# Performance work log

Hardware: AMD Instinct MI355X
Metric: run time of the kernel (lower is better)

## Reference

```python
import jax, jax.numpy as jnp
import numpy as np

# RosaAttention config constants
H = 16       # num_rosa_heads
KV = 4       # num_rosa_key_value_heads
QKB = 64     # num_rosa_query_key_bits
VB = 64      # num_rosa_value_bits
HID = 2048   # hidden_size
TAU = 1.0    # temperature buffer


def setup_inputs() -> dict:
    key = jax.random.key(0)
    ks = jax.random.split(key, 8)
    B, S = 2, 2048
    sc = 0.02
    return {
        "x": jax.random.normal(ks[0], (B, S, HID), jnp.float32),
        "attention_mask": jnp.ones((B, S), jnp.int32),
        "Wq": jax.random.normal(ks[1], (HID, H * QKB), jnp.float32) * sc,
        "Wk": jax.random.normal(ks[2], (HID, KV * QKB), jnp.float32) * sc,
        "Wv": jax.random.normal(ks[3], (HID, KV * VB), jnp.float32) * sc,
        "Wo": jax.random.normal(ks[4], (H * VB, HID), jnp.float32) * sc,
        "emb0": jnp.full((H, VB), -1e-05, jnp.float32),
        "emb1": jnp.full((H, VB), +1e-05, jnp.float32),
    }


def reference(x, attention_mask, Wq, Wk, Wv, Wo, emb0, emb1):
    B, S, _ = x.shape
    rep = H // KV
    # projections -> [b, s, heads, bits]
    xq = (x @ Wq).reshape(B, S, H, QKB)
    xk = (x @ Wk).reshape(B, S, KV, QKB)
    xv = (x @ Wv).reshape(B, S, KV, VB)
    # repeat_kv: each kv head repeated n_rep times contiguously
    xk = jnp.repeat(xk, rep, axis=2)   # [b, s, H, QKB]
    xv = jnp.repeat(xv, rep, axis=2)   # [b, s, H, VB]
    # soft bit quantization of q/k, tau-scaled bit-similarity score
    qb = jnp.tanh(xq)
    kb = jnp.tanh(xk)
    scores = jnp.einsum('bqhd,bkhd->bhqk', qb, kb) / (TAU * QKB)
    # causal mask + padding mask (mask True = attend)
    causal = jnp.tril(jnp.ones((S, S), bool))
    mask = causal[None, None] & attention_mask.astype(bool)[:, None, None, :]
    scores = jnp.where(mask, scores, jnp.finfo(scores.dtype).min)
    probs = jax.nn.softmax(scores, axis=-1)        # [b, h, q, k]
    # soft-binarized values: per-bit probabilities, attended, then mapped
    # through learned per-head bit embeddings emb0 (bit=0) / emb1 (bit=1)
    vp = jax.nn.sigmoid(xv)                        # [b, s, H, VB]
    ctx = jnp.einsum('bhqk,bkhv->bqhv', probs, vp) # [b, s, H, VB]
    out_bits = ctx * emb1[None, None] + (1.0 - ctx) * emb0[None, None]
    out = out_bits.reshape(B, S, H * VB) @ Wo      # [b, s, HID]
    return out
```

## Files before the change

kernel.cpp:

```cpp
#include <hip/hip_runtime.h>
#include <math.h>

typedef short bf16x8 __attribute__((ext_vector_type(8)));
typedef float f32x4 __attribute__((ext_vector_type(4)));
typedef unsigned int u32x2 __attribute__((ext_vector_type(2)));
typedef unsigned int u32x4 __attribute__((ext_vector_type(4)));

#define MFMA_BF16(A,B,C) __builtin_amdgcn_mfma_f32_16x16x32_bf16(A,B,C,0,0,0)

#define VMCNT(N) asm volatile("s_waitcnt vmcnt(" #N ")" ::: "memory")
#define LGKM0()  asm volatile("s_waitcnt lgkmcnt(0)" ::: "memory")
#define RBAR() do { asm volatile("" ::: "memory"); __builtin_amdgcn_s_barrier(); \
                    asm volatile("" ::: "memory"); } while (0)

__device__ __forceinline__ unsigned short f2b(float x) {
    union { float f; unsigned int u; } v; v.f = x;
    unsigned int r = v.u + 0x7FFFu + ((v.u >> 16) & 1u);
    return (unsigned short)(r >> 16);
}

__device__ __forceinline__ unsigned int cvtpk(float lo, float hi) {
    unsigned int r;
    asm("v_cvt_pk_bf16_f32 %0, %1, %2" : "=v"(r) : "v"(lo), "v"(hi));
    return r;
}

__device__ __forceinline__ void gload16(const unsigned short* g, unsigned short* l) {
    __builtin_amdgcn_global_load_lds(
        (const __attribute__((address_space(1))) unsigned int*)(g),
        (__attribute__((address_space(3))) unsigned int*)(l),
        16, 0, 0);
}

__global__ __launch_bounds__(256) void conv_bf16(const float* __restrict__ s,
                                                 unsigned short* __restrict__ d, int n)
{
    int i = blockIdx.x * blockDim.x + threadIdx.x;
    int stride = gridDim.x * blockDim.x;
    for (int idx = i * 4; idx < n; idx += stride * 4) {
        float4 v = *(const float4*)(s + idx);
        ushort4 o;
        o.x = f2b(v.x); o.y = f2b(v.y); o.z = f2b(v.z); o.w = f2b(v.w);
        *(ushort4*)(d + idx) = o;
    }
}

__global__ __launch_bounds__(256) void transp_conv_qkv(const float* __restrict__ Wq,
                                                       const float* __restrict__ Wk,
                                                       const float* __restrict__ Wv,
                                                       unsigned short* __restrict__ dst)
{
    __shared__ float t[32][33];
    const int tx = threadIdx.x, ty = threadIdx.y;
    int bx = blockIdx.x;
    const float* src; int C, cb, dco;
    if (bx < 32)      { src = Wq; C = 1024; cb = bx;      dco = 0; }
    else if (bx < 40) { src = Wk; C = 256;  cb = bx - 32; dco = 1024; }
    else              { src = Wv; C = 256;  cb = bx - 40; dco = 1280; }
    const int c = cb * 32 + tx;
    const int r0 = blockIdx.y * 32;
#pragma unroll
    for (int i = 0; i < 4; ++i)
        t[ty + i * 8][tx] = src[(size_t)(r0 + ty + i * 8) * C + c];
    __syncthreads();
    const int cc = cb * 32 + ty;
#pragma unroll
    for (int i = 0; i < 4; ++i)
        dst[(size_t)(dco + cc + i * 8) * 2048 + r0 + tx] = f2b(t[tx][ty + i * 8]);
}

__global__ __launch_bounds__(256) void transp_conv(const float* __restrict__ src, int R, int C,
                                                   unsigned short* __restrict__ dst, int pitch)
{
    __shared__ float t[32][33];
    const int tx = threadIdx.x, ty = threadIdx.y;
    const int c = blockIdx.x * 32 + tx;
    const int r0 = blockIdx.y * 32;
#pragma unroll
    for (int i = 0; i < 4; ++i)
        t[ty + i * 8][tx] = src[(size_t)(r0 + ty + i * 8) * C + c];
    __syncthreads();
    const int cc = blockIdx.x * 32 + ty;
#pragma unroll
    for (int i = 0; i < 4; ++i)
        dst[(size_t)(cc + i * 8) * pitch + r0 + tx] = f2b(t[tx][ty + i * 8]);
}

__device__ __forceinline__ void stage_g(const unsigned short* AgL, const unsigned short* BgL,
                                        int K, int k0s,
                                        unsigned short* Asb, unsigned short* Bsb, int w)
{
#pragma unroll
    for (int t = 0; t < 4; ++t) {
        const int sub = t >> 1, half = t & 1;
        gload16(AgL + (size_t)(half * 16) * K + k0s + sub * 32,
                Asb + sub * 4096 + (w * 2 + half) * 512);
    }
#pragma unroll
    for (int kk = 0; kk < 2; ++kk)
        gload16(BgL + k0s + kk * 32, Bsb + kk * 2048 + w * 512);
}

template <int MODE>
__global__ __launch_bounds__(256, 3) void gemm_bt_mfma(
    const unsigned short* __restrict__ A,
    const unsigned short* __restrict__ Bt,
    int M, int N, int K,
    float* __restrict__ Cf,
    unsigned short* __restrict__ qh,
    unsigned short* __restrict__ kh,
    unsigned short* __restrict__ vtt)
{
    __shared__ __align__(16) unsigned short As[2][2 * 128 * 32];
    __shared__ __align__(16) unsigned short Bs[2][2 * 64 * 32];

    const int tid = threadIdx.x;
    const int w = tid >> 6, lane = tid & 63, l15 = lane & 15, quad = lane >> 4;
    const int wm = w & 1, wn = w >> 1;
    const int m0 = blockIdx.y * 128, n0 = blockIdx.x * 64;

    const int dsrow = lane >> 2;
    const int dscol = ((lane & 3) ^ ((lane >> 3) & 3)) * 8;
    const int sl8   = (((lane & 15) << 2) | ((lane >> 4) ^ ((lane >> 1) & 3))) * 8;

    f32x4 acc[4][2];
    const f32x4 zero4 = {0.f, 0.f, 0.f, 0.f};
#pragma unroll
    for (int i = 0; i < 4; ++i)
#pragma unroll
        for (int j = 0; j < 2; ++j) acc[i][j] = zero4;

    const unsigned short* AgL = A  + (size_t)(m0 + w * 32 + dsrow) * K + dscol;
    const unsigned short* BgL = Bt + (size_t)(n0 + w * 16 + dsrow) * K + dscol;

    const int NT = K >> 6;
    stage_g(AgL, BgL, K, 0, &As[0][0], &Bs[0][0], w);

    int cb = 0;
    for (int t = 0; t < NT; ++t) {
        if (t + 1 < NT) {
            stage_g(AgL, BgL, K, (t + 1) * 64, &As[cb ^ 1][0], &Bs[cb ^ 1][0], w);
            VMCNT(6);
        } else {
            VMCNT(0);
        }
        RBAR();

        bf16x8 af[4][2], bf[2][2];
#pragma unroll
        for (int kk = 0; kk < 2; ++kk) {
#pragma unroll
            for (int mt = 0; mt < 4; ++mt)
                af[mt][kk] = *(const bf16x8*)&As[cb][kk * 4096 + (wm * 4 + mt) * 512 + sl8];
#pragma unroll
            for (int nt = 0; nt < 2; ++nt)
                bf[nt][kk] = *(const bf16x8*)&Bs[cb][kk * 2048 + (wn * 2 + nt) * 512 + sl8];
        }
#pragma unroll
        for (int kk = 0; kk < 2; ++kk)
#pragma unroll
            for (int mt = 0; mt < 4; ++mt)
#pragma unroll
                for (int nt = 0; nt < 2; ++nt)
                    acc[mt][nt] = MFMA_BF16(af[mt][kk], bf[nt][kk], acc[mt][nt]);

        if (t + 1 < NT) RBAR();
        cb ^= 1;
    }

    if (MODE == 0) {
#pragma unroll
        for (int mt = 0; mt < 4; ++mt)
#pragma unroll
            for (int nt = 0; nt < 2; ++nt) {
                const int gn = n0 + wn * 32 + nt * 16 + l15;
#pragma unroll
                for (int r = 0; r < 4; ++r) {
                    const int gm = m0 + wm * 64 + mt * 16 + quad * 4 + r;
                    Cf[(size_t)gm * N + gn] = acc[mt][nt][r];
                }
            }
    } else {
        if (n0 < 1024) {
#pragma unroll
            for (int mt = 0; mt < 4; ++mt)
#pragma unroll
                for (int nt = 0; nt < 2; ++nt) {
                    const int gn = n0 + wn * 32 + nt * 16 + l15;
#pragma unroll
                    for (int r = 0; r < 4; ++r) {
                        const int gm = m0 + wm * 64 + mt * 16 + quad * 4 + r;
                        qh[(size_t)gm * 1024 + gn] = f2b(tanhf(acc[mt][nt][r]));
                    }
                }
        } else if (n0 < 1280) {
#pragma unroll
            for (int mt = 0; mt < 4; ++mt)
#pragma unroll
                for (int nt = 0; nt < 2; ++nt) {
                    const int gn = n0 + wn * 32 + nt * 16 + l15 - 1024;
#pragma unroll
                    for (int r = 0; r < 4; ++r) {
                        const int gm = m0 + wm * 64 + mt * 16 + quad * 4 + r;
                        kh[(size_t)gm * 256 + gn] = f2b(tanhf(acc[mt][nt][r]));
                    }
                }
        } else {
#pragma unroll
            for (int mt = 0; mt < 4; ++mt)
#pragma unroll
                for (int nt = 0; nt < 2; ++nt) {
                    const int gn = n0 + wn * 32 + nt * 16 + l15 - 1280;
                    const int g = gn >> 6, vv = gn & 63;
                    const int s0 = m0 + wm * 64 + mt * 16 + quad * 4;
                    const int b = s0 >> 11, sl = s0 & 2047;
                    ushort4 pk;
                    unsigned short* pp = (unsigned short*)&pk;
#pragma unroll
                    for (int r = 0; r < 4; ++r) {
                        float sv = 1.0f / (1.0f + __expf(-acc[mt][nt][r]));
                        pp[r] = f2b(sv);
                    }
                    *(ushort4*)&vtt[((size_t)(b * 4 + g) * 64 + vv) * 2048 + sl] = pk;
                }
        }
    }
}

__global__ __launch_bounds__(256, 4) void rosa_attn_mfma(
    const unsigned short* __restrict__ qh,
    const unsigned short* __restrict__ kh,
    const unsigned short* __restrict__ vtt,
    const int* __restrict__ amask,
    const float* __restrict__ emb0,
    const float* __restrict__ emb1,
    unsigned short* __restrict__ ob)
{
    __shared__ __align__(16) unsigned short Ks[2][2][2048];
    __shared__ __align__(16) unsigned short Vs[2][2][2048];
    __shared__ __align__(16) unsigned int   Ps[4][16][32];

    const int a = blockIdx.x & 7, m = blockIdx.x >> 3;
    const int h = blockIdx.y, b = blockIdx.z, g = h >> 2;
    const int hb = h + 16 * b;
    const int sel = (m + (hb >> 3)) & 3;
    const int qt = (sel == 0) ? a : (sel == 1) ? 15 - a : (sel == 2) ? 16 + a : 31 - a;

    const int tid = threadIdx.x;
    const int w = tid >> 6, lane = tid & 63, l15 = lane & 15, quad = lane >> 4;

    const int dsrow = lane >> 2;
    const int dscol = ((lane & 3) ^ ((lane >> 3) & 3)) * 8;
    const int sl8   = (((lane & 15) << 2) | ((lane >> 4) ^ ((lane >> 1) & 3))) * 8;
    const int pxor  = (l15 & 7) << 2;

    const unsigned short* kst = kh + (size_t)b * 2048 * 256 + g * 64
                               + (size_t)(w * 16 + dsrow) * 256 + dscol;
    const unsigned short* vst = vtt + ((size_t)(b * 4 + g) * 64 + w * 16 + dsrow) * 2048
                               + dscol;
    const int* mbase = amask + b * 2048;

    const f32x4 zero4 = {0.f, 0.f, 0.f, 0.f};
    const float cexp = 0.0225421100f;

    float cm[4];
#pragma unroll
    for (int r = 0; r < 4; ++r) cm[r] = (quad * 4 + r <= l15) ? 1.0f : 0.0f;

    const int4 mv0 = *(const int4*)(mbase + tid * 8);
    const int4 mv1 = *(const int4*)(mbase + tid * 8 + 4);

    const int q0 = qt * 64;
    const int nkt = qt + 1;

    const unsigned short* qrow = qh + ((size_t)(b * 2048 + q0 + w * 16 + l15) * 16 + h) * 64;
    const bf16x8 qf0 = *(const bf16x8*)(qrow + quad * 8);
    const bf16x8 qf1 = *(const bf16x8*)(qrow + 32 + quad * 8);

#define STAGE_TILE(k0s, buf)                                               \
    {                                                                      \
        gload16(kst + (size_t)(k0s) * 256,      &Ks[buf][0][w * 512]);     \
        gload16(kst + (size_t)(k0s) * 256 + 32, &Ks[buf][1][w * 512]);     \
        gload16(vst + (k0s),                    &Vs[buf][0][w * 512]);     \
        gload16(vst + (k0s) + 32,               &Vs[buf][1][w * 512]);     \
    }

    STAGE_TILE(0, 0)

    const bool f8 = mv0.x && mv0.y && mv0.z && mv0.w && mv1.x && mv1.y && mv1.z && mv1.w;
    const unsigned long long bal = __ballot(f8);
    const bool bytefull = ((bal >> ((lane & 7) * 8)) & 0xFFull) == 0xFFull;
    const unsigned long long bal2 = __ballot(bytefull && (lane < 8));
    if (lane == 0) Ps[0][0][w] = (unsigned int)(bal2 & 0xFFull);
    RBAR();
    const unsigned int mflags = Ps[0][0][0] | (Ps[0][0][1] << 8)
                              | (Ps[0][0][2] << 16) | (Ps[0][0][3] << 24);
    LGKM0();
    RBAR();

    f32x4 oacc[4];
#pragma unroll
    for (int t = 0; t < 4; ++t) oacc[t] = zero4;
    float psum = 0.0f;

    int cb = 0;
    for (int kt = 0; kt < nkt; ++kt) {
        if (kt + 1 < nkt) {
            STAGE_TILE((kt + 1) * 64, cb ^ 1)
            VMCNT(4);
        } else {
            VMCNT(0);
        }
        RBAR();

        const int k0 = kt * 64;
        const bool diag = (kt == qt);
        const bool full = (mflags >> kt) & 1u;
        const int ntlim = diag ? (w + 1) : 4;

#pragma unroll
        for (int nt = 0; nt < 4; ++nt) {
            u32x2 pk2;
            if (nt < ntlim) {
                bf16x8 kf0 = *(const bf16x8*)&Ks[cb][0][nt * 512 + sl8];
                bf16x8 kf1 = *(const bf16x8*)&Ks[cb][1][nt * 512 + sl8];
                __builtin_amdgcn_s_setprio(1);
                f32x4 sc = MFMA_BF16(kf0, qf0, zero4);
                sc = MFMA_BF16(kf1, qf1, sc);
                __builtin_amdgcn_s_setprio(0);
                const bool dnw = diag && (nt == w);
                float p[4];
                if (full) {
                    if (dnw) {
#pragma unroll
                        for (int r = 0; r < 4; ++r)
                            p[r] = __builtin_exp2f(sc[r] * cexp) * cm[r];
                    } else {
#pragma unroll
                        for (int r = 0; r < 4; ++r)
                            p[r] = __builtin_exp2f(sc[r] * cexp);
                    }
                } else {
                    const int4 m4 = *(const int4*)(mbase + k0 + nt * 16 + quad * 4);
                    const int* mm = (const int*)&m4;
#pragma unroll
                    for (int r = 0; r < 4; ++r) {
                        float pv = __builtin_exp2f(sc[r] * cexp);
                        if (dnw) pv *= cm[r];
                        p[r] = (mm[r] != 0) ? pv : 0.0f;
                    }
                }
                psum += (p[0] + p[1]) + (p[2] + p[3]);
                pk2[0] = cvtpk(p[0], p[1]);
                pk2[1] = cvtpk(p[2], p[3]);
            } else {
                pk2[0] = 0u; pk2[1] = 0u;
            }
            *(u32x2*)&Ps[w][l15][(nt * 8 + quad * 2) ^ pxor] = pk2;
        }

        const bf16x8 pf0 = __builtin_bit_cast(bf16x8, *(const u32x4*)&Ps[w][l15][(quad * 4) ^ pxor]);
        const bf16x8 pf1 = __builtin_bit_cast(bf16x8, *(const u32x4*)&Ps[w][l15][(16 + quad * 4) ^ pxor]);
        __builtin_amdgcn_s_setprio(1);
#pragma unroll
        for (int nt = 0; nt < 4; ++nt) {
            bf16x8 vf0 = *(const bf16x8*)&Vs[cb][0][nt * 512 + sl8];
            bf16x8 vf1 = *(const bf16x8*)&Vs[cb][1][nt * 512 + sl8];
            oacc[nt] = MFMA_BF16(pf0, vf0, oacc[nt]);
            oacc[nt] = MFMA_BF16(pf1, vf1, oacc[nt]);
        }
        __builtin_amdgcn_s_setprio(0);

        if (kt + 1 < nkt) {
            RBAR();
            cb ^= 1;
        }
    }

    float l = psum;
    l += __shfl_xor(l, 16);
    l += __shfl_xor(l, 32);
    float lq[4];
#pragma unroll
    for (int r = 0; r < 4; ++r) lq[r] = __shfl(l, quad * 4 + r);

#pragma unroll
    for (int nt = 0; nt < 4; ++nt) {
        const float e0 = emb0[h * 64 + nt * 16 + l15];
        const float e1 = emb1[h * 64 + nt * 16 + l15];
#pragma unroll
        for (int r = 0; r < 4; ++r) {
            const float ctx = oacc[nt][r] / lq[r];
            const float val = e0 + ctx * (e1 - e0);
            const size_t s_idx = (size_t)(b * 2048 + q0 + w * 16 + quad * 4 + r);
            ob[(s_idx * 16 + h) * 64 + nt * 16 + l15] = f2b(val);
        }
    }
#undef STAGE_TILE
}

extern "C" void kernel_launch(void* const* d_in, const int* in_sizes, int n_in,
                              void* d_out, int out_size, void* d_ws, size_t ws_size,
                              hipStream_t stream)
{
    const float* x    = (const float*)d_in[0];
    const int*   amask= (const int*)d_in[1];
    const float* Wq   = (const float*)d_in[2];
    const float* Wk   = (const float*)d_in[3];
    const float* Wv   = (const float*)d_in[4];
    const float* Wo   = (const float*)d_in[5];
    const float* emb0 = (const float*)d_in[6];
    const float* emb1 = (const float*)d_in[7];
    float* out = (float*)d_out;

    char* base = (char*)d_ws;
    unsigned short* xh    = (unsigned short*)(base);
    unsigned short* ob    = xh;
    unsigned short* Wqkvt = (unsigned short*)(base + (16u << 20));
    unsigned short* Wot   = (unsigned short*)(base + (22u << 20));
    unsigned short* qh    = (unsigned short*)(base + (26u << 20));
    unsigned short* kh    = (unsigned short*)(base + (34u << 20));
    unsigned short* vtt   = (unsigned short*)(base + (36u << 20));

    conv_bf16<<<2048, 256, 0, stream>>>(x, xh, 4096 * 2048);
    transp_conv_qkv<<<dim3(48, 64), dim3(32, 8), 0, stream>>>(Wq, Wk, Wv, Wqkvt);
    transp_conv<<<dim3(64, 32), dim3(32, 8), 0, stream>>>(Wo, 1024, 2048, Wot, 1024);

    gemm_bt_mfma<1><<<dim3(24, 32), 256, 0, stream>>>(xh, Wqkvt, 4096, 1536, 2048,
                                                      nullptr, qh, kh, vtt);
    rosa_attn_mfma<<<dim3(32, 16, 2), 256, 0, stream>>>(qh, kh, vtt, amask, emb0, emb1, ob);
    gemm_bt_mfma<0><<<dim3(32, 32), 256, 0, stream>>>(ob, Wot, 4096, 2048, 1024,
                                                      out, nullptr, nullptr, nullptr);
}
```

Baseline: 229.8 us.

## Switch attention to 32x32x16 MFMA tiles with in-register P transpose and split-K reduction

Result: faster. 223.6 us (-2.7%).

```diff
diff --git a/kernel.cpp b/kernel.cpp
--- a/kernel.cpp
+++ b/kernel.cpp
@@ -3,15 +3,17 @@
 
 typedef short bf16x8 __attribute__((ext_vector_type(8)));
 typedef float f32x4 __attribute__((ext_vector_type(4)));
+typedef float f32x16 __attribute__((ext_vector_type(16)));
 typedef unsigned int u32x2 __attribute__((ext_vector_type(2)));
 typedef unsigned int u32x4 __attribute__((ext_vector_type(4)));
 
 #define MFMA_BF16(A,B,C) __builtin_amdgcn_mfma_f32_16x16x32_bf16(A,B,C,0,0,0)
+#define MFMA32(A,B,C)    __builtin_amdgcn_mfma_f32_32x32x16_bf16(A,B,C,0,0,0)
 
 #define VMCNT(N) asm volatile("s_waitcnt vmcnt(" #N ")" ::: "memory")
-#define LGKM0()  asm volatile("s_waitcnt lgkmcnt(0)" ::: "memory")
 #define RBAR() do { asm volatile("" ::: "memory"); __builtin_amdgcn_s_barrier(); \
                     asm volatile("" ::: "memory"); } while (0)
+#define PERMSWAP(a, b) asm volatile("v_permlane32_swap_b32 %0, %1" : "+v"(a), "+v"(b))
 
 __device__ __forceinline__ unsigned short f2b(float x) {
     union { float f; unsigned int u; } v; v.f = x;
@@ -190,7 +192,7 @@
 #pragma unroll
                     for (int r = 0; r < 4; ++r) {
                         const int gm = m0 + wm * 64 + mt * 16 + quad * 4 + r;
-                        qh[(size_t)gm * 1024 + gn] = f2b(tanhf(acc[mt][nt][r]));
+                        qh[(size_t)gm * 1024 + gn] = f2b(tanhf(acc[mt][nt][r]) * 0.0225421100f);
                     }
                 }
         } else if (n0 < 1280) {
@@ -236,9 +238,10 @@
     const float* __restrict__ emb1,
     unsigned short* __restrict__ ob)
 {
-    __shared__ __align__(16) unsigned short Ks[2][2][2048];
-    __shared__ __align__(16) unsigned short Vs[2][2][2048];
-    __shared__ __align__(16) unsigned int   Ps[4][16][32];
+    __shared__ __align__(16) unsigned short Ks[2][4096];
+    __shared__ __align__(16) unsigned short Vs[2][4096];
+    __shared__ unsigned int Mflg[4];
+    __shared__ float Lred[2][2][32];
 
     const int a = blockIdx.x & 7, m = blockIdx.x >> 3;
     const int h = blockIdx.y, b = blockIdx.z, g = h >> 2;
@@ -247,61 +250,67 @@
     const int qt = (sel == 0) ? a : (sel == 1) ? 15 - a : (sel == 2) ? 16 + a : 31 - a;
 
     const int tid = threadIdx.x;
-    const int w = tid >> 6, lane = tid & 63, l15 = lane & 15, quad = lane >> 4;
-
-    const int dsrow = lane >> 2;
-    const int dscol = ((lane & 3) ^ ((lane >> 3) & 3)) * 8;
-    const int sl8   = (((lane & 15) << 2) | ((lane >> 4) ^ ((lane >> 1) & 3))) * 8;
-    const int pxor  = (l15 & 7) << 2;
-
-    const unsigned short* kst = kh + (size_t)b * 2048 * 256 + g * 64
-                               + (size_t)(w * 16 + dsrow) * 256 + dscol;
-    const unsigned short* vst = vtt + ((size_t)(b * 4 + g) * 64 + w * 16 + dsrow) * 2048
-                               + dscol;
+    const int w = tid >> 6, lane = tid & 63;
+    const int kq = w >> 1, qq = w & 1;
+    const int l31 = lane & 31, H = lane >> 5, x7 = lane & 7;
+
+    const int srow = lane >> 3;
+    const int scol = ((lane & 7) ^ srow) * 8;
+    const unsigned short* kst0 = kh + ((size_t)(b * 2048) + w * 16 + srow) * 256 + g * 64 + scol;
+    const unsigned short* vst0 = vtt + ((size_t)(b * 4 + g) * 64 + w * 16 + srow) * 2048 + scol;
     const int* mbase = amask + b * 2048;
 
-    const f32x4 zero4 = {0.f, 0.f, 0.f, 0.f};
-    const float cexp = 0.0225421100f;
-
-    float cm[4];
-#pragma unroll
-    for (int r = 0; r < 4; ++r) cm[r] = (quad * 4 + r <= l15) ? 1.0f : 0.0f;
+    int kadr[4];
+#pragma unroll
+    for (int mi = 0; mi < 4; ++mi)
+        kadr[mi] = (kq * 32 + l31) * 64 + (((mi * 2 + H) ^ x7) * 8);
+    int vadr[2][2];
+#pragma unroll
+    for (int vh = 0; vh < 2; ++vh)
+#pragma unroll
+        for (int kc = 0; kc < 2; ++kc)
+            vadr[vh][kc] = (vh * 32 + l31) * 64 + (((kq * 4 + kc * 2 + H) ^ x7) * 8);
+
+    unsigned int cbits = 0;
+#pragma unroll
+    for (int r = 0; r < 16; ++r) {
+        const int kl = (r & 3) + 8 * (r >> 2) + 4 * H;
+        if (kl <= l31) cbits |= (1u << r);
+    }
+
+    const int q0 = qt * 64, nkt = qt + 1;
+
+#define STAGE_TILE(k0s, buf)                                                   \
+    {                                                                          \
+        gload16(kst0 + (size_t)(k0s) * 256,        &Ks[buf][(w * 16) * 64]);   \
+        gload16(kst0 + (size_t)(k0s) * 256 + 2048, &Ks[buf][(w * 16 + 8) * 64]);\
+        gload16(vst0 + (k0s),                      &Vs[buf][(w * 16) * 64]);   \
+        gload16(vst0 + (k0s) + 16384,              &Vs[buf][(w * 16 + 8) * 64]);\
+    }
 
     const int4 mv0 = *(const int4*)(mbase + tid * 8);
     const int4 mv1 = *(const int4*)(mbase + tid * 8 + 4);
 
-    const int q0 = qt * 64;
-    const int nkt = qt + 1;
-
-    const unsigned short* qrow = qh + ((size_t)(b * 2048 + q0 + w * 16 + l15) * 16 + h) * 64;
-    const bf16x8 qf0 = *(const bf16x8*)(qrow + quad * 8);
-    const bf16x8 qf1 = *(const bf16x8*)(qrow + 32 + quad * 8);
-
-#define STAGE_TILE(k0s, buf)                                               \
-    {                                                                      \
-        gload16(kst + (size_t)(k0s) * 256,      &Ks[buf][0][w * 512]);     \
-        gload16(kst + (size_t)(k0s) * 256 + 32, &Ks[buf][1][w * 512]);     \
-        gload16(vst + (k0s),                    &Vs[buf][0][w * 512]);     \
-        gload16(vst + (k0s) + 32,               &Vs[buf][1][w * 512]);     \
-    }
-
     STAGE_TILE(0, 0)
+
+    const unsigned short* qp = qh + ((size_t)(b * 2048 + q0 + qq * 32 + l31) * 16 + h) * 64 + H * 8;
+    const bf16x8 qf0 = *(const bf16x8*)(qp);
+    const bf16x8 qf1 = *(const bf16x8*)(qp + 16);
+    const bf16x8 qf2 = *(const bf16x8*)(qp + 32);
+    const bf16x8 qf3 = *(const bf16x8*)(qp + 48);
 
     const bool f8 = mv0.x && mv0.y && mv0.z && mv0.w && mv1.x && mv1.y && mv1.z && mv1.w;
     const unsigned long long bal = __ballot(f8);
     const bool bytefull = ((bal >> ((lane & 7) * 8)) & 0xFFull) == 0xFFull;
     const unsigned long long bal2 = __ballot(bytefull && (lane < 8));
-    if (lane == 0) Ps[0][0][w] = (unsigned int)(bal2 & 0xFFull);
+    if (lane == 0) Mflg[w] = (unsigned int)(bal2 & 0xFFull);
     RBAR();
-    const unsigned int mflags = Ps[0][0][0] | (Ps[0][0][1] << 8)
-                              | (Ps[0][0][2] << 16) | (Ps[0][0][3] << 24);
-    LGKM0();
-    RBAR();
-
-    f32x4 oacc[4];
-#pragma unroll
-    for (int t = 0; t < 4; ++t) oacc[t] = zero4;
+    const unsigned int mflags = Mflg[0] | (Mflg[1] << 8) | (Mflg[2] << 16) | (Mflg[3] << 24);
+
+    const f32x16 z16 = {0.f,0.f,0.f,0.f, 0.f,0.f,0.f,0.f, 0.f,0.f,0.f,0.f, 0.f,0.f,0.f,0.f};
+    f32x16 oacc0 = z16, oacc1 = z16;
     float psum = 0.0f;
+    const bool skipdiag = (kq > qq);
 
     int cb = 0;
     for (int kt = 0; kt < nkt; ++kt) {
@@ -313,88 +322,110 @@
         }
         RBAR();
 
-        const int k0 = kt * 64;
         const bool diag = (kt == qt);
-        const bool full = (mflags >> kt) & 1u;
-        const int ntlim = diag ? (w + 1) : 4;
-
-#pragma unroll
-        for (int nt = 0; nt < 4; ++nt) {
-            u32x2 pk2;
-            if (nt < ntlim) {
-                bf16x8 kf0 = *(const bf16x8*)&Ks[cb][0][nt * 512 + sl8];
-                bf16x8 kf1 = *(const bf16x8*)&Ks[cb][1][nt * 512 + sl8];
-                __builtin_amdgcn_s_setprio(1);
-                f32x4 sc = MFMA_BF16(kf0, qf0, zero4);
-                sc = MFMA_BF16(kf1, qf1, sc);
-                __builtin_amdgcn_s_setprio(0);
-                const bool dnw = diag && (nt == w);
-                float p[4];
-                if (full) {
-                    if (dnw) {
-#pragma unroll
-                        for (int r = 0; r < 4; ++r)
-                            p[r] = __builtin_exp2f(sc[r] * cexp) * cm[r];
-                    } else {
-#pragma unroll
-                        for (int r = 0; r < 4; ++r)
-                            p[r] = __builtin_exp2f(sc[r] * cexp);
-                    }
-                } else {
-                    const int4 m4 = *(const int4*)(mbase + k0 + nt * 16 + quad * 4);
-                    const int* mm = (const int*)&m4;
-#pragma unroll
-                    for (int r = 0; r < 4; ++r) {
-                        float pv = __builtin_exp2f(sc[r] * cexp);
-                        if (dnw) pv *= cm[r];
-                        p[r] = (mm[r] != 0) ? pv : 0.0f;
-                    }
+        if (!(diag && skipdiag)) {
+            const bf16x8 kf0 = *(const bf16x8*)&Ks[cb][kadr[0]];
+            const bf16x8 kf1 = *(const bf16x8*)&Ks[cb][kadr[1]];
+            const bf16x8 kf2 = *(const bf16x8*)&Ks[cb][kadr[2]];
+            const bf16x8 kf3 = *(const bf16x8*)&Ks[cb][kadr[3]];
+            __builtin_amdgcn_s_setprio(1);
+            f32x16 sc = MFMA32(kf0, qf0, z16);
+            sc = MFMA32(kf1, qf1, sc);
+            sc = MFMA32(kf2, qf2, sc);
+            sc = MFMA32(kf3, qf3, sc);
+            __builtin_amdgcn_s_setprio(0);
+
+            float p[16];
+#pragma unroll
+            for (int r = 0; r < 16; ++r) p[r] = __builtin_exp2f(sc[r]);
+            if (diag && kq == qq) {
+#pragma unroll
+                for (int r = 0; r < 16; ++r)
+                    if (!((cbits >> r) & 1u)) p[r] = 0.0f;
+            }
+            if (!((mflags >> kt) & 1u)) {
+#pragma unroll
+                for (int r = 0; r < 16; ++r) {
+                    const int kgl = kt * 64 + kq * 32 + (r & 3) + 8 * (r >> 2) + 4 * H;
+                    if (mbase[kgl] == 0) p[r] = 0.0f;
                 }
-                psum += (p[0] + p[1]) + (p[2] + p[3]);
-                pk2[0] = cvtpk(p[0], p[1]);
-                pk2[1] = cvtpk(p[2], p[3]);
-            } else {
-                pk2[0] = 0u; pk2[1] = 0u;
             }
-            *(u32x2*)&Ps[w][l15][(nt * 8 + quad * 2) ^ pxor] = pk2;
-        }
-
-        const bf16x8 pf0 = __builtin_bit_cast(bf16x8, *(const u32x4*)&Ps[w][l15][(quad * 4) ^ pxor]);
-        const bf16x8 pf1 = __builtin_bit_cast(bf16x8, *(const u32x4*)&Ps[w][l15][(16 + quad * 4) ^ pxor]);
-        __builtin_amdgcn_s_setprio(1);
-#pragma unroll
-        for (int nt = 0; nt < 4; ++nt) {
-            bf16x8 vf0 = *(const bf16x8*)&Vs[cb][0][nt * 512 + sl8];
-            bf16x8 vf1 = *(const bf16x8*)&Vs[cb][1][nt * 512 + sl8];
-            oacc[nt] = MFMA_BF16(pf0, vf0, oacc[nt]);
-            oacc[nt] = MFMA_BF16(pf1, vf1, oacc[nt]);
-        }
-        __builtin_amdgcn_s_setprio(0);
-
-        if (kt + 1 < nkt) {
-            RBAR();
-            cb ^= 1;
-        }
-    }
-
-    float l = psum;
-    l += __shfl_xor(l, 16);
-    l += __shfl_xor(l, 32);
-    float lq[4];
-#pragma unroll
-    for (int r = 0; r < 4; ++r) lq[r] = __shfl(l, quad * 4 + r);
-
-#pragma unroll
-    for (int nt = 0; nt < 4; ++nt) {
-        const float e0 = emb0[h * 64 + nt * 16 + l15];
-        const float e1 = emb1[h * 64 + nt * 16 + l15];
-#pragma unroll
-        for (int r = 0; r < 4; ++r) {
-            const float ctx = oacc[nt][r] / lq[r];
-            const float val = e0 + ctx * (e1 - e0);
-            const size_t s_idx = (size_t)(b * 2048 + q0 + w * 16 + quad * 4 + r);
-            ob[(s_idx * 16 + h) * 64 + nt * 16 + l15] = f2b(val);
-        }
+            psum += (((p[0]+p[1])+(p[2]+p[3])) + ((p[4]+p[5])+(p[6]+p[7])))
+                  + (((p[8]+p[9])+(p[10]+p[11])) + ((p[12]+p[13])+(p[14]+p[15])));
+
+            unsigned int W0 = cvtpk(p[0],  p[1]),  W1 = cvtpk(p[2],  p[3]);
+            unsigned int W2 = cvtpk(p[4],  p[5]),  W3 = cvtpk(p[6],  p[7]);
+            unsigned int W4 = cvtpk(p[8],  p[9]),  W5 = cvtpk(p[10], p[11]);
+            unsigned int W6 = cvtpk(p[12], p[13]), W7 = cvtpk(p[14], p[15]);
+            PERMSWAP(W0, W2);  PERMSWAP(W1, W3);
+            PERMSWAP(W4, W6);  PERMSWAP(W5, W7);
+            u32x4 paw0; paw0[0] = W0; paw0[1] = W1; paw0[2] = W2; paw0[3] = W3;
+            u32x4 paw1; paw1[0] = W4; paw1[1] = W5; paw1[2] = W6; paw1[3] = W7;
+            const bf16x8 pa0 = __builtin_bit_cast(bf16x8, paw0);
+            const bf16x8 pa1 = __builtin_bit_cast(bf16x8, paw1);
+
+            const bf16x8 vb00 = *(const bf16x8*)&Vs[cb][vadr[0][0]];
+            const bf16x8 vb01 = *(const bf16x8*)&Vs[cb][vadr[0][1]];
+            const bf16x8 vb10 = *(const bf16x8*)&Vs[cb][vadr[1][0]];
+            const bf16x8 vb11 = *(const bf16x8*)&Vs[cb][vadr[1][1]];
+            __builtin_amdgcn_s_setprio(1);
+            oacc0 = MFMA32(pa0, vb00, oacc0);
+            oacc0 = MFMA32(pa1, vb01, oacc0);
+            oacc1 = MFMA32(pa0, vb10, oacc1);
+            oacc1 = MFMA32(pa1, vb11, oacc1);
+            __builtin_amdgcn_s_setprio(0);
+        }
+
+        if (kt + 1 < nkt) { RBAR(); cb ^= 1; }
+    }
+
+    psum += __shfl_xor(psum, 32);
+
+    RBAR();
+
+    if (H == 0) Lred[kq][qq][l31] = psum;
+
+    float* Ored = (float*)&Ks[0][0];
+    const int slw = qq * 2 + (1 - kq);
+    if (kq == 0) {
+#pragma unroll
+        for (int c = 0; c < 4; ++c) {
+            float4 t = {oacc1[c*4+0], oacc1[c*4+1], oacc1[c*4+2], oacc1[c*4+3]};
+            *(float4*)&Ored[slw * 1024 + lane * 16 + ((c ^ (lane & 3)) * 4)] = t;
+        }
+    } else {
+#pragma unroll
+        for (int c = 0; c < 4; ++c) {
+            float4 t = {oacc0[c*4+0], oacc0[c*4+1], oacc0[c*4+2], oacc0[c*4+3]};
+            *(float4*)&Ored[slw * 1024 + lane * 16 + ((c ^ (lane & 3)) * 4)] = t;
+        }
+    }
+    RBAR();
+
+    const int slr = qq * 2 + kq;
+    f32x16 osum = (kq == 0) ? oacc0 : oacc1;
+#pragma unroll
+    for (int c = 0; c < 4; ++c) {
+        float4 t = *(const float4*)&Ored[slr * 1024 + lane * 16 + ((c ^ (lane & 3)) * 4)];
+        osum[c*4+0] += t.x; osum[c*4+1] += t.y; osum[c*4+2] += t.z; osum[c*4+3] += t.w;
+    }
+
+    float rl[16];
+#pragma unroll
+    for (int r = 0; r < 16; ++r) {
+        const int ql = (r & 3) + 8 * (r >> 2) + 4 * H;
+        rl[r] = __builtin_amdgcn_rcpf(Lred[0][qq][ql] + Lred[1][qq][ql]);
+    }
+
+    const int vg = kq * 32 + l31;
+    const float e0 = emb0[h * 64 + vg];
+    const float ed = emb1[h * 64 + vg] - e0;
+    unsigned short* obp = ob + ((size_t)(b * 2048 + q0 + qq * 32) * 16 + h) * 64 + vg;
+#pragma unroll
+    for (int r = 0; r < 16; ++r) {
+        const int ql = (r & 3) + 8 * (r >> 2) + 4 * H;
+        const float val = e0 + (osum[r] * rl[r]) * ed;
+        obp[(size_t)ql * 1024] = f2b(val);
     }
 #undef STAGE_TILE
 }
```
